# Kernel optimization log

Measured on AMD Instinct MI355X. Metric: run time of the kernel, lower is better.

## Reference

```python
import jax, jax.numpy as jnp
import numpy as np

B, T, C, H = 2, 2048, 1024, 16
D = C // H  # head dim = 64

def setup_inputs() -> dict:
    key = jax.random.key(0)
    ks = jax.random.split(key, 5)
    s = 0.02
    return {
        "x": jax.random.normal(ks[0], (B, T, C), dtype=jnp.float32),
        "Wqkv": jax.random.normal(ks[1], (C, 3 * C), dtype=jnp.float32) * s,
        "bqkv": jnp.zeros((3 * C,), dtype=jnp.float32),
        "Wproj": jax.random.normal(ks[2], (C, C), dtype=jnp.float32) * s,
        "bproj": jnp.zeros((C,), dtype=jnp.float32),
    }

def reference(x, Wqkv, bqkv, Wproj, bproj):
    b, t, c = x.shape
    qkv = x @ Wqkv + bqkv                       # [B,T,3C]
    q, k, v = jnp.split(qkv, 3, axis=-1)
    # [B,T,C] -> [B,H,T,D]
    q = q.reshape(b, t, H, D).transpose(0, 2, 1, 3)
    k = k.reshape(b, t, H, D).transpose(0, 2, 1, 3)
    v = v.reshape(b, t, H, D).transpose(0, 2, 1, 3)
    scale = 1.0 / np.sqrt(D).astype(np.float32)
    attn = jnp.einsum('bhqd,bhkd->bhqk', q, k) * scale  # [B,H,T,T]
    causal = jnp.tril(jnp.ones((t, t), dtype=bool))
    attn = jnp.where(causal, attn, jnp.float32(-jnp.inf))
    attn = jax.nn.softmax(attn, axis=-1)
    y = jnp.einsum('bhqk,bhkd->bhqd', attn, v)          # [B,H,T,D]
    y = y.transpose(0, 2, 1, 3).reshape(b, t, c)        # [B,T,C]
    return y @ Wproj + bproj
```

## Files before the change

kernel.cpp:

```cpp
#include <hip/hip_runtime.h>
#include <stdint.h>

#define B_ 2
#define T_ 2048
#define C_ 1024
#define H_ 16
#define D_ 64
#define M_ (B_*T_)
#define BHTD_ (B_*H_*T_*D_)

typedef __bf16 bf16x8 __attribute__((ext_vector_type(8)));
typedef __bf16 bf16x4 __attribute__((ext_vector_type(4)));
typedef float f32x4 __attribute__((ext_vector_type(4)));

static __device__ __forceinline__ unsigned short f32_bf16(float f) {
    unsigned int u = __float_as_uint(f);
    u += 0x7FFFu + ((u >> 16) & 1u);
    return (unsigned short)(u >> 16);
}

__global__ void prep_kernel(const float* __restrict__ x, unsigned short* __restrict__ xbf,
                            const float* __restrict__ Wqkv, unsigned short* __restrict__ wqkv_t,
                            const float* __restrict__ Wproj, unsigned short* __restrict__ wproj_t) {
    __shared__ float tile[32][33];
    const int id = blockIdx.x;
    const int tid = threadIdx.x;
    if (id < 4096) {
        int i = (id * 256 + tid) * 4;
        float4 f = *(const float4*)(x + i);
        ushort4 o;
        o.x = f32_bf16(f.x); o.y = f32_bf16(f.y); o.z = f32_bf16(f.z); o.w = f32_bf16(f.w);
        *(ushort4*)(xbf + i) = o;
        return;
    }
    const float* W; unsigned short* Wt; int K, N, bx, by;
    if (id < 7168) {
        int r = id - 4096; W = Wqkv; Wt = wqkv_t; K = 1024; N = 3072;
        bx = r % 96; by = r / 96;
    } else {
        int r = id - 7168; W = Wproj; Wt = wproj_t; K = 1024; N = 1024;
        bx = r & 31; by = r >> 5;
    }
    int n0 = bx * 32, k0 = by * 32;
    int tx = tid & 31, ty = tid >> 5;
    #pragma unroll
    for (int j = 0; j < 32; j += 8)
        tile[ty + j][tx] = W[(size_t)(k0 + ty + j) * N + n0 + tx];
    __syncthreads();
    #pragma unroll
    for (int j = 0; j < 32; j += 8)
        Wt[(size_t)(n0 + ty + j) * K + k0 + tx] = f32_bf16(tile[tx][ty + j]);
}

template<int EPI, int BN>
__global__ __launch_bounds__(256) void gemm_bt(
    const unsigned short* __restrict__ A,
    const unsigned short* __restrict__ Bt,
    const float* __restrict__ bias,
    unsigned short* __restrict__ out_bf16,
    float* __restrict__ out_f32,
    int M, int N, int K)
{
    constexpr int NI = (BN == 128) ? 4 : 2;
    constexpr int BSTR = BN * 32;
    __shared__ __align__(16) unsigned short smem[16640];
    unsigned short* AsU = smem;
    unsigned short* BsU = smem + 8192;
    int tid = threadIdx.x;
    int lane = tid & 63, wid = tid >> 6;
    int fr = lane & 15, fg = lane >> 4;
    int row0 = blockIdx.x * 128, col0 = blockIdx.y * BN;
    int wm = (wid >> 1) * 64, wn = (wid & 1) * (BN / 2);

    f32x4 acc[4][NI];
    #pragma unroll
    for (int i = 0; i < 4; ++i)
        #pragma unroll
        for (int j = 0; j < NI; ++j)
            acc[i][j] = (f32x4){0.f, 0.f, 0.f, 0.f};

    const int srw = lane >> 2;
    const int scl = (lane & 3) * 8;
    const int c0 = wid * 2, c1 = wid * 2 + 1;

    auto stage = [&](int buf, int k0) {
        __builtin_amdgcn_global_load_lds(
            (const __attribute__((address_space(1))) void*)(A + (size_t)(row0 + c0 * 16 + srw) * K + k0 + scl),
            (__attribute__((address_space(3))) void*)(AsU + buf * 4096 + c0 * 512), 16, 0, 0);
        __builtin_amdgcn_global_load_lds(
            (const __attribute__((address_space(1))) void*)(A + (size_t)(row0 + c1 * 16 + srw) * K + k0 + scl),
            (__attribute__((address_space(3))) void*)(AsU + buf * 4096 + c1 * 512), 16, 0, 0);
        if (BN == 128) {
            __builtin_amdgcn_global_load_lds(
                (const __attribute__((address_space(1))) void*)(Bt + (size_t)(col0 + c0 * 16 + srw) * K + k0 + scl),
                (__attribute__((address_space(3))) void*)(BsU + buf * BSTR + c0 * 512), 16, 0, 0);
            __builtin_amdgcn_global_load_lds(
                (const __attribute__((address_space(1))) void*)(Bt + (size_t)(col0 + c1 * 16 + srw) * K + k0 + scl),
                (__attribute__((address_space(3))) void*)(BsU + buf * BSTR + c1 * 512), 16, 0, 0);
        } else {
            __builtin_amdgcn_global_load_lds(
                (const __attribute__((address_space(1))) void*)(Bt + (size_t)(col0 + wid * 16 + srw) * K + k0 + scl),
                (__attribute__((address_space(3))) void*)(BsU + buf * BSTR + wid * 512), 16, 0, 0);
        }
    };

    stage(0, 0);
    __syncthreads();

    int cur = 0;
    for (int k0 = 0; k0 < K; k0 += 32) {
        if (k0 + 32 < K) stage(cur ^ 1, k0 + 32);

        bf16x8 af[4], bfr[NI];
        #pragma unroll
        for (int i = 0; i < 4; ++i)
            af[i] = *(const bf16x8*)(AsU + cur * 4096 + (wm + i * 16 + fr) * 32 + fg * 8);
        #pragma unroll
        for (int i = 0; i < NI; ++i)
            bfr[i] = *(const bf16x8*)(BsU + cur * BSTR + (wn + i * 16 + fr) * 32 + fg * 8);
        #pragma unroll
        for (int mi = 0; mi < 4; ++mi)
            #pragma unroll
            for (int ni = 0; ni < NI; ++ni)
                acc[mi][ni] = __builtin_amdgcn_mfma_f32_16x16x32_bf16(af[mi], bfr[ni], acc[mi][ni], 0, 0, 0);

        __syncthreads();
        cur ^= 1;
    }

    if (EPI == 0 && BN == 128 && col0 >= 2048) {
        #pragma unroll
        for (int ni = 0; ni < NI; ++ni) {
            const int cl = wn + ni * 16 + fr;
            const float bv = bias[col0 + cl];
            #pragma unroll
            for (int mi = 0; mi < 4; ++mi) {
                const int rl = wm + mi * 16 + fg * 4;
                bf16x4 pk = {(__bf16)(acc[mi][ni][0] + bv), (__bf16)(acc[mi][ni][1] + bv),
                             (__bf16)(acc[mi][ni][2] + bv), (__bf16)(acc[mi][ni][3] + bv)};
                uint2 w = __builtin_bit_cast(uint2, pk);
                *(unsigned int*)(smem + cl * 130 + rl)     = w.x;
                *(unsigned int*)(smem + cl * 130 + rl + 2) = w.y;
            }
        }
        __syncthreads();
        const int c = tid >> 1, half = tid & 1;
        const int col = col0 + c;
        const int d = col & 63, h2 = (col >> 6) & 15;
        const int bb = row0 >> 11;
        const int t0 = (row0 & 2047) + half * 64;
        unsigned short* dst = out_bf16 + (size_t)2 * BHTD_ +
                              ((size_t)(bb * H_ + h2) * D_ + d) * T_ + t0;
        const unsigned short* src = smem + c * 130 + half * 64;
        #pragma unroll
        for (int j = 0; j < 8; ++j) {
            uint4 v;
            v.x = *(const unsigned int*)(src + j * 8 + 0);
            v.y = *(const unsigned int*)(src + j * 8 + 2);
            v.z = *(const unsigned int*)(src + j * 8 + 4);
            v.w = *(const unsigned int*)(src + j * 8 + 6);
            *(uint4*)(dst + j * 8) = v;
        }
        return;
    }

    #pragma unroll
    for (int mi = 0; mi < 4; ++mi) {
        int rowb = row0 + wm + mi * 16 + fg * 4;
        #pragma unroll
        for (int ni = 0; ni < NI; ++ni) {
            int col = col0 + wn + ni * 16 + fr;
            float bv = bias[col];
            #pragma unroll
            for (int r = 0; r < 4; ++r) {
                float v = acc[mi][ni][r] + bv;
                int rr = rowb + r;
                if (EPI == 0) {
                    int part = col >> 10, c = col & 1023;
                    int h = c >> 6, d = c & 63;
                    int b = rr >> 11, t = rr & 2047;
                    if (part == 0) v *= 0.18033688011112042f;
                    size_t idx = (size_t)part * BHTD_ + ((size_t)(b * H_ + h) * T_ + t) * D_ + d;
                    out_bf16[idx] = f32_bf16(v);
                } else {
                    out_f32[(size_t)rr * N + col] = v;
                }
            }
        }
    }
}

__global__ __launch_bounds__(256) void attn_kernel(
    const unsigned short* __restrict__ qg,
    const unsigned short* __restrict__ kg,
    const unsigned short* __restrict__ vtg,
    unsigned short* __restrict__ y)
{
    const int id = blockIdx.x;
    const int xcd = id & 7, loc = id >> 3;
    const int bh = xcd * 4 + (loc & 3);
    const int iq0 = loc >> 2;
    const int iq = (iq0 < 8) ? iq0 : 23 - iq0;
    const int chlo = iq, chhi = 31 - iq;
    const int b = bh >> 4, h = bh & 15;
    const int tid = threadIdx.x, wid = tid >> 6, lane = tid & 63;
    const int fr = lane & 15, fg = lane >> 4;

    const unsigned short* qp = qg + (size_t)bh * (T_ * D_);
    const unsigned short* kp = kg + (size_t)bh * (T_ * D_);
    const unsigned short* vp = vtg + (size_t)bh * (D_ * T_);

    __shared__ __align__(16) char Ks[2][64 * 128];
    __shared__ __align__(16) char Vs[2][64 * 128];
    __shared__ __align__(16) char Ps[4][32 * 128];
    char* Pw = Ps[wid];

    const int rhi = chhi * 64 + wid * 16;
    const int rlo = chlo * 64 + wid * 16;

    const int srow = tid >> 3;
    const int scb  = (tid & 7) * 16;
    const int sws  = scb ^ ((srow & 7) << 4);

    bf16x8 qhi[2], qlo[2];
    #pragma unroll
    for (int kd = 0; kd < 2; ++kd) {
        qhi[kd] = *(const bf16x8*)(qp + (size_t)(rhi + fr) * D_ + kd * 32 + fg * 8);
        qlo[kd] = *(const bf16x8*)(qp + (size_t)(rlo + fr) * D_ + kd * 32 + fg * 8);
    }

    f32x4 oHi[4], oLo[4];
    float lHi = 0.f, lLo = 0.f;
    #pragma unroll
    for (int n = 0; n < 4; ++n) {
        oHi[n] = (f32x4){0.f, 0.f, 0.f, 0.f};
        oLo[n] = (f32x4){0.f, 0.f, 0.f, 0.f};
    }

    const int ntk  = chhi + 1;
    const int ntlo = chlo + 1;

    {
        uint4 k0 = *(const uint4*)(kp + (size_t)srow        * D_ + (scb >> 1));
        uint4 k1 = *(const uint4*)(kp + (size_t)(srow + 32) * D_ + (scb >> 1));
        uint4 v0 = *(const uint4*)(vp + (size_t)srow        * T_ + (scb >> 1));
        uint4 v1 = *(const uint4*)(vp + (size_t)(srow + 32) * T_ + (scb >> 1));
        *(uint4*)(Ks[0] + srow * 128 + sws)        = k0;
        *(uint4*)(Ks[0] + (srow + 32) * 128 + sws) = k1;
        *(uint4*)(Vs[0] + srow * 128 + sws)        = v0;
        *(uint4*)(Vs[0] + (srow + 32) * 128 + sws) = v1;
    }
    __syncthreads();

    int cur = 0;
    for (int t = 0; t < ntk; ++t) {
        const int kv0 = t * 64;
        const int kv1 = (t + 1 < ntk) ? kv0 + 64 : kv0;

        uint4 pk0 = *(const uint4*)(kp + (size_t)(kv1 + srow)      * D_ + (scb >> 1));
        uint4 pk1 = *(const uint4*)(kp + (size_t)(kv1 + srow + 32) * D_ + (scb >> 1));
        uint4 pv0 = *(const uint4*)(vp + (size_t)srow        * T_ + kv1 + (scb >> 1));
        uint4 pv1 = *(const uint4*)(vp + (size_t)(srow + 32) * T_ + kv1 + (scb >> 1));

        const char* Kb = Ks[cur];
        const char* Vb = Vs[cur];
        const unsigned lsw = (unsigned)((fr & 7) << 4);
        const bool lo_act = (t < ntlo);

        f32x4 sh[4], sl[4];
        #pragma unroll
        for (int n = 0; n < 4; ++n) {
            sh[n] = (f32x4){0.f, 0.f, 0.f, 0.f};
            sl[n] = (f32x4){0.f, 0.f, 0.f, 0.f};
        }
        __builtin_amdgcn_s_setprio(1);
        #pragma unroll
        for (int kd = 0; kd < 2; ++kd)
            #pragma unroll
            for (int n = 0; n < 4; ++n) {
                bf16x8 kf = *(const bf16x8*)(Kb + (n * 16 + fr) * 128 +
                                             (((unsigned)(kd * 64 + fg * 16)) ^ lsw));
                sh[n] = __builtin_amdgcn_mfma_f32_16x16x32_bf16(kf, qhi[kd], sh[n], 0, 0, 0);
                if (lo_act)
                    sl[n] = __builtin_amdgcn_mfma_f32_16x16x32_bf16(kf, qlo[kd], sl[n], 0, 0, 0);
            }
        __builtin_amdgcn_s_setprio(0);

        bf16x8 vf[4][2];
        #pragma unroll
        for (int nd = 0; nd < 4; ++nd)
            #pragma unroll
            for (int kk = 0; kk < 2; ++kk)
                vf[nd][kk] = *(const bf16x8*)(Vb + (nd * 16 + fr) * 128 +
                                              (((unsigned)(kk * 64 + fg * 16)) ^ lsw));

        {
            const bool masked = (t == chhi);
            const int qrow = rhi + fr;
            const unsigned prow = (unsigned)fr * 128;
            #pragma unroll
            for (int n = 0; n < 4; ++n) {
                float x0 = sh[n][0], x1 = sh[n][1], x2 = sh[n][2], x3 = sh[n][3];
                if (masked) {
                    const int kvb = kv0 + n * 16 + fg * 4;
                    if (kvb     > qrow) x0 = -1e30f;
                    if (kvb + 1 > qrow) x1 = -1e30f;
                    if (kvb + 2 > qrow) x2 = -1e30f;
                    if (kvb + 3 > qrow) x3 = -1e30f;
                }
                const float p0 = exp2f(x0), p1 = exp2f(x1);
                const float p2 = exp2f(x2), p3 = exp2f(x3);
                lHi += (p0 + p1) + (p2 + p3);
                bf16x4 pk4 = {(__bf16)p0, (__bf16)p1, (__bf16)p2, (__bf16)p3};
                *(uint2*)(Pw + ((prow + (unsigned)(n * 32 + fg * 8)) ^ lsw)) =
                    __builtin_bit_cast(uint2, pk4);
            }
        }
        {
            const unsigned prow = (unsigned)fr * 128;
            __builtin_amdgcn_s_setprio(1);
            #pragma unroll
            for (int kk = 0; kk < 2; ++kk) {
                bf16x8 pb = *(const bf16x8*)(Pw + ((prow + (unsigned)(kk * 64 + fg * 16)) ^ lsw));
                #pragma unroll
                for (int nd = 0; nd < 4; ++nd)
                    oHi[nd] = __builtin_amdgcn_mfma_f32_16x16x32_bf16(vf[nd][kk], pb, oHi[nd], 0, 0, 0);
            }
            __builtin_amdgcn_s_setprio(0);
        }
        if (lo_act) {
            const bool masked = (t == chlo);
            const int qrow = rlo + fr;
            const unsigned prow = (unsigned)(16 + fr) * 128;
            #pragma unroll
            for (int n = 0; n < 4; ++n) {
                float x0 = sl[n][0], x1 = sl[n][1], x2 = sl[n][2], x3 = sl[n][3];
                if (masked) {
                    const int kvb = kv0 + n * 16 + fg * 4;
                    if (kvb     > qrow) x0 = -1e30f;
                    if (kvb + 1 > qrow) x1 = -1e30f;
                    if (kvb + 2 > qrow) x2 = -1e30f;
                    if (kvb + 3 > qrow) x3 = -1e30f;
                }
                const float p0 = exp2f(x0), p1 = exp2f(x1);
                const float p2 = exp2f(x2), p3 = exp2f(x3);
                lLo += (p0 + p1) + (p2 + p3);
                bf16x4 pk4 = {(__bf16)p0, (__bf16)p1, (__bf16)p2, (__bf16)p3};
                *(uint2*)(Pw + ((prow + (unsigned)(n * 32 + fg * 8)) ^ lsw)) =
                    __builtin_bit_cast(uint2, pk4);
            }
            const unsigned prow2 = (unsigned)(16 + fr) * 128;
            __builtin_amdgcn_s_setprio(1);
            #pragma unroll
            for (int kk = 0; kk < 2; ++kk) {
                bf16x8 pb = *(const bf16x8*)(Pw + ((prow2 + (unsigned)(kk * 64 + fg * 16)) ^ lsw));
                #pragma unroll
                for (int nd = 0; nd < 4; ++nd)
                    oLo[nd] = __builtin_amdgcn_mfma_f32_16x16x32_bf16(vf[nd][kk], pb, oLo[nd], 0, 0, 0);
            }
            __builtin_amdgcn_s_setprio(0);
        }

        {
            char* Kn = Ks[cur ^ 1];
            char* Vn = Vs[cur ^ 1];
            *(uint4*)(Kn + srow * 128 + sws)        = pk0;
            *(uint4*)(Kn + (srow + 32) * 128 + sws) = pk1;
            *(uint4*)(Vn + srow * 128 + sws)        = pv0;
            *(uint4*)(Vn + (srow + 32) * 128 + sws) = pv1;
        }
        __syncthreads();
        cur ^= 1;
    }

    #pragma unroll
    for (int s = 0; s < 2; ++s) {
        float rs = s ? lLo : lHi;
        rs += __shfl_xor(rs, 16);
        rs += __shfl_xor(rs, 32);
        const float inv = 1.f / rs;
        const int trow = (s ? rlo : rhi) + fr;
        f32x4* oT = s ? oLo : oHi;
        #pragma unroll
        for (int nd = 0; nd < 4; ++nd) {
            bf16x4 ov = {(__bf16)(oT[nd][0] * inv), (__bf16)(oT[nd][1] * inv),
                         (__bf16)(oT[nd][2] * inv), (__bf16)(oT[nd][3] * inv)};
            *(uint2*)(y + ((size_t)b * T_ + trow) * C_ + h * 64 + nd * 16 + fg * 4) =
                __builtin_bit_cast(uint2, ov);
        }
    }
}

extern "C" void kernel_launch(void* const* d_in, const int* in_sizes, int n_in,
                              void* d_out, int out_size, void* d_ws, size_t ws_size,
                              hipStream_t stream) {
    const float* x     = (const float*)d_in[0];
    const float* Wqkv  = (const float*)d_in[1];
    const float* bqkv  = (const float*)d_in[2];
    const float* Wproj = (const float*)d_in[3];
    const float* bproj = (const float*)d_in[4];
    float* out = (float*)d_out;

    char* ws = (char*)d_ws;
    unsigned short* x_bf    = (unsigned short*)(ws);
    unsigned short* wqkv_t  = (unsigned short*)(ws + 8388608);
    unsigned short* wproj_t = (unsigned short*)(ws + 14680064);
    unsigned short* qkv     = (unsigned short*)(ws + 16777216);
    unsigned short* ybuf    = (unsigned short*)(ws + 41943040);

    prep_kernel<<<dim3(8192), 256, 0, stream>>>(x, x_bf, Wqkv, wqkv_t, Wproj, wproj_t);

    gemm_bt<0, 128><<<dim3(M_ / 128, 3072 / 128), 256, 0, stream>>>(
        x_bf, wqkv_t, bqkv, qkv, nullptr, M_, 3072, 1024);

    attn_kernel<<<dim3(512), 256, 0, stream>>>(
        qkv, qkv + (size_t)BHTD_, qkv + 2 * (size_t)BHTD_, ybuf);

    gemm_bt<1, 64><<<dim3(M_ / 128, 1024 / 64), 256, 0, stream>>>(
        ybuf, wproj_t, bproj, nullptr, out, M_, 1024, 1024);
}
```

Before: 119.5 us.

## Rewrite attention with 32x32 MFMA, register P via permlane swap, direct-to-LDS loads

The attention kernel moves from 16x16x32 MFMA tiles to 32x32x16 MFMA tiles. P is kept in registers and rearranged with permlane32_swap instead of a round trip through shared memory. K/V staging now uses global_load_lds so tiles go straight into LDS without passing through registers, and the block shrinks to 128 threads with two waves each covering 32 query rows. The query-tile ordering also changes. This aims to cut LDS traffic and register staging, at the cost of fewer waves per block and possibly lower occupancy.

```diff
diff --git a/kernel.cpp b/kernel.cpp
--- a/kernel.cpp
+++ b/kernel.cpp
@@ -11,12 +11,19 @@
 
 typedef __bf16 bf16x8 __attribute__((ext_vector_type(8)));
 typedef __bf16 bf16x4 __attribute__((ext_vector_type(4)));
+typedef __bf16 bf16x2 __attribute__((ext_vector_type(2)));
 typedef float f32x4 __attribute__((ext_vector_type(4)));
+typedef float f32x16 __attribute__((ext_vector_type(16)));
 
 static __device__ __forceinline__ unsigned short f32_bf16(float f) {
     unsigned int u = __float_as_uint(f);
     u += 0x7FFFu + ((u >> 16) & 1u);
     return (unsigned short)(u >> 16);
+}
+
+static __device__ __forceinline__ int pack_bf16_2(float a, float b) {
+    bf16x2 v = {(__bf16)a, (__bf16)b};
+    return __builtin_bit_cast(int, v);
 }
 
 __global__ void prep_kernel(const float* __restrict__ x, unsigned short* __restrict__ xbf,
@@ -190,7 +197,7 @@
     }
 }
 
-__global__ __launch_bounds__(256) void attn_kernel(
+__global__ __launch_bounds__(128, 1) void attn_kernel(
     const unsigned short* __restrict__ qg,
     const unsigned short* __restrict__ kg,
     const unsigned short* __restrict__ vtg,
@@ -199,194 +206,185 @@
     const int id = blockIdx.x;
     const int xcd = id & 7, loc = id >> 3;
     const int bh = xcd * 4 + (loc & 3);
-    const int iq0 = loc >> 2;
-    const int iq = (iq0 < 8) ? iq0 : 23 - iq0;
-    const int chlo = iq, chhi = 31 - iq;
+    const int iq = loc >> 2;
+    const int chhi = 31 - iq, chlo = iq;
     const int b = bh >> 4, h = bh & 15;
     const int tid = threadIdx.x, wid = tid >> 6, lane = tid & 63;
-    const int fr = lane & 15, fg = lane >> 4;
+    const int lq = lane & 31, hi = lane >> 5;
 
     const unsigned short* qp = qg + (size_t)bh * (T_ * D_);
-    const unsigned short* kp = kg + (size_t)bh * (T_ * D_);
-    const unsigned short* vp = vtg + (size_t)bh * (D_ * T_);
-
-    __shared__ __align__(16) char Ks[2][64 * 128];
-    __shared__ __align__(16) char Vs[2][64 * 128];
-    __shared__ __align__(16) char Ps[4][32 * 128];
-    char* Pw = Ps[wid];
-
-    const int rhi = chhi * 64 + wid * 16;
-    const int rlo = chlo * 64 + wid * 16;
-
-    const int srow = tid >> 3;
-    const int scb  = (tid & 7) * 16;
-    const int sws  = scb ^ ((srow & 7) << 4);
-
-    bf16x8 qhi[2], qlo[2];
-    #pragma unroll
-    for (int kd = 0; kd < 2; ++kd) {
-        qhi[kd] = *(const bf16x8*)(qp + (size_t)(rhi + fr) * D_ + kd * 32 + fg * 8);
-        qlo[kd] = *(const bf16x8*)(qp + (size_t)(rlo + fr) * D_ + kd * 32 + fg * 8);
-    }
-
-    f32x4 oHi[4], oLo[4];
-    float lHi = 0.f, lLo = 0.f;
-    #pragma unroll
-    for (int n = 0; n < 4; ++n) {
-        oHi[n] = (f32x4){0.f, 0.f, 0.f, 0.f};
-        oLo[n] = (f32x4){0.f, 0.f, 0.f, 0.f};
-    }
-
-    const int ntk  = chhi + 1;
-    const int ntlo = chlo + 1;
-
-    {
-        uint4 k0 = *(const uint4*)(kp + (size_t)srow        * D_ + (scb >> 1));
-        uint4 k1 = *(const uint4*)(kp + (size_t)(srow + 32) * D_ + (scb >> 1));
-        uint4 v0 = *(const uint4*)(vp + (size_t)srow        * T_ + (scb >> 1));
-        uint4 v1 = *(const uint4*)(vp + (size_t)(srow + 32) * T_ + (scb >> 1));
-        *(uint4*)(Ks[0] + srow * 128 + sws)        = k0;
-        *(uint4*)(Ks[0] + (srow + 32) * 128 + sws) = k1;
-        *(uint4*)(Vs[0] + srow * 128 + sws)        = v0;
-        *(uint4*)(Vs[0] + (srow + 32) * 128 + sws) = v1;
-    }
+    const char* kpB = (const char*)(kg + (size_t)bh * (T_ * D_));
+    const char* vpB = (const char*)(vtg + (size_t)bh * (D_ * T_));
+
+    __shared__ __align__(16) char Ks[2][8192];
+    __shared__ __align__(16) char Vs[2][8192];
+
+    const int rhi = chhi * 64 + wid * 32;
+    const int rlo = chlo * 64 + wid * 32;
+    const int ntk = chhi + 1, ntlo = chlo + 1;
+
+    bf16x8 qh[4], ql[4];
+    #pragma unroll
+    for (int ds = 0; ds < 4; ++ds) {
+        qh[ds] = *(const bf16x8*)(qp + (size_t)(rhi + lq) * D_ + ds * 16 + hi * 8);
+        ql[ds] = *(const bf16x8*)(qp + (size_t)(rlo + lq) * D_ + ds * 16 + hi * 8);
+    }
+
+    f32x16 oh0, oh1, ol0, ol1;
+    #pragma unroll
+    for (int e = 0; e < 16; ++e) { oh0[e] = 0.f; oh1[e] = 0.f; ol0[e] = 0.f; ol1[e] = 0.f; }
+    float lh = 0.f, ll = 0.f;
+
+    const int srow8 = lane >> 3;
+    const int scol  = (lane & 7) * 16;
+    const int ssw   = srow8 << 4;
+
+    auto stage = [&](int buf, int kv0) {
+        #pragma unroll
+        for (int blk = 0; blk < 4; ++blk) {
+            const int rbase = wid * 32 + blk * 8;
+            __builtin_amdgcn_global_load_lds(
+                (const __attribute__((address_space(1))) void*)
+                    (kpB + (size_t)(kv0 + rbase + srow8) * 128 + (scol ^ ssw)),
+                (__attribute__((address_space(3))) void*)(Ks[buf] + rbase * 128), 16, 0, 0);
+            __builtin_amdgcn_global_load_lds(
+                (const __attribute__((address_space(1))) void*)
+                    (vpB + (size_t)(rbase + srow8) * 4096 + kv0 * 2 + (scol ^ ssw)),
+                (__attribute__((address_space(3))) void*)(Vs[buf] + rbase * 128), 16, 0, 0);
+        }
+    };
+
+    auto make_pb = [&](const f32x16& p4, int g4a) -> bf16x8 {
+        int A0 = pack_bf16_2(p4[g4a * 4 + 0], p4[g4a * 4 + 1]);
+        int A1 = pack_bf16_2(p4[g4a * 4 + 2], p4[g4a * 4 + 3]);
+        int B0 = pack_bf16_2(p4[g4a * 4 + 4], p4[g4a * 4 + 5]);
+        int B1 = pack_bf16_2(p4[g4a * 4 + 6], p4[g4a * 4 + 7]);
+        auto ra = __builtin_amdgcn_permlane32_swap(A0, B0, false, false);
+        auto rb = __builtin_amdgcn_permlane32_swap(A1, B1, false, false);
+        int4 w;
+        w.x = ra[0]; w.y = rb[0]; w.z = ra[1]; w.w = rb[1];
+        return __builtin_bit_cast(bf16x8, w);
+    };
+
+    stage(0, 0);
     __syncthreads();
 
+    const int lsw = (lq & 7) << 4;
     int cur = 0;
     for (int t = 0; t < ntk; ++t) {
         const int kv0 = t * 64;
-        const int kv1 = (t + 1 < ntk) ? kv0 + 64 : kv0;
-
-        uint4 pk0 = *(const uint4*)(kp + (size_t)(kv1 + srow)      * D_ + (scb >> 1));
-        uint4 pk1 = *(const uint4*)(kp + (size_t)(kv1 + srow + 32) * D_ + (scb >> 1));
-        uint4 pv0 = *(const uint4*)(vp + (size_t)srow        * T_ + kv1 + (scb >> 1));
-        uint4 pv1 = *(const uint4*)(vp + (size_t)(srow + 32) * T_ + kv1 + (scb >> 1));
+        if (t + 1 < ntk) stage(cur ^ 1, kv0 + 64);
 
         const char* Kb = Ks[cur];
         const char* Vb = Vs[cur];
-        const unsigned lsw = (unsigned)((fr & 7) << 4);
         const bool lo_act = (t < ntlo);
 
-        f32x4 sh[4], sl[4];
-        #pragma unroll
-        for (int n = 0; n < 4; ++n) {
-            sh[n] = (f32x4){0.f, 0.f, 0.f, 0.f};
-            sl[n] = (f32x4){0.f, 0.f, 0.f, 0.f};
-        }
-        __builtin_amdgcn_s_setprio(1);
-        #pragma unroll
-        for (int kd = 0; kd < 2; ++kd)
-            #pragma unroll
-            for (int n = 0; n < 4; ++n) {
-                bf16x8 kf = *(const bf16x8*)(Kb + (n * 16 + fr) * 128 +
-                                             (((unsigned)(kd * 64 + fg * 16)) ^ lsw));
-                sh[n] = __builtin_amdgcn_mfma_f32_16x16x32_bf16(kf, qhi[kd], sh[n], 0, 0, 0);
-                if (lo_act)
-                    sl[n] = __builtin_amdgcn_mfma_f32_16x16x32_bf16(kf, qlo[kd], sl[n], 0, 0, 0);
-            }
-        __builtin_amdgcn_s_setprio(0);
-
-        bf16x8 vf[4][2];
-        #pragma unroll
-        for (int nd = 0; nd < 4; ++nd)
-            #pragma unroll
-            for (int kk = 0; kk < 2; ++kk)
-                vf[nd][kk] = *(const bf16x8*)(Vb + (nd * 16 + fr) * 128 +
-                                              (((unsigned)(kk * 64 + fg * 16)) ^ lsw));
+        f32x16 sh0, sh1, sl0, sl1;
+        #pragma unroll
+        for (int e = 0; e < 16; ++e) { sh0[e] = 0.f; sh1[e] = 0.f; sl0[e] = 0.f; sl1[e] = 0.f; }
+        #pragma unroll
+        for (int ds = 0; ds < 4; ++ds) {
+            bf16x8 kfA = *(const bf16x8*)(Kb + lq * 128        + ((ds * 32 + hi * 16) ^ lsw));
+            bf16x8 kfB = *(const bf16x8*)(Kb + (32 + lq) * 128 + ((ds * 32 + hi * 16) ^ lsw));
+            sh0 = __builtin_amdgcn_mfma_f32_32x32x16_bf16(kfA, qh[ds], sh0, 0, 0, 0);
+            sh1 = __builtin_amdgcn_mfma_f32_32x32x16_bf16(kfB, qh[ds], sh1, 0, 0, 0);
+            if (lo_act) {
+                sl0 = __builtin_amdgcn_mfma_f32_32x32x16_bf16(kfA, ql[ds], sl0, 0, 0, 0);
+                sl1 = __builtin_amdgcn_mfma_f32_32x32x16_bf16(kfB, ql[ds], sl1, 0, 0, 0);
+            }
+        }
+
+        bf16x8 vf[2][4];
+        #pragma unroll
+        for (int dd = 0; dd < 2; ++dd)
+            #pragma unroll
+            for (int st = 0; st < 4; ++st)
+                vf[dd][st] = *(const bf16x8*)(Vb + (dd * 32 + lq) * 128 +
+                                              ((st * 32 + hi * 16) ^ lsw));
 
         {
-            const bool masked = (t == chhi);
-            const int qrow = rhi + fr;
-            const unsigned prow = (unsigned)fr * 128;
-            #pragma unroll
-            for (int n = 0; n < 4; ++n) {
-                float x0 = sh[n][0], x1 = sh[n][1], x2 = sh[n][2], x3 = sh[n][3];
-                if (masked) {
-                    const int kvb = kv0 + n * 16 + fg * 4;
-                    if (kvb     > qrow) x0 = -1e30f;
-                    if (kvb + 1 > qrow) x1 = -1e30f;
-                    if (kvb + 2 > qrow) x2 = -1e30f;
-                    if (kvb + 3 > qrow) x3 = -1e30f;
+            const bool diag = (t == chhi);
+            const int qrow = rhi + lq;
+            if (diag) {
+                #pragma unroll
+                for (int e = 0; e < 16; ++e) {
+                    const int kvl = (e & 3) + ((e >> 2) << 3) + hi * 4;
+                    sh0[e] = exp2f((kv0 + kvl <= qrow) ? sh0[e] : -1e30f);
+                    sh1[e] = exp2f((kv0 + 32 + kvl <= qrow) ? sh1[e] : -1e30f);
                 }
-                const float p0 = exp2f(x0), p1 = exp2f(x1);
-                const float p2 = exp2f(x2), p3 = exp2f(x3);
-                lHi += (p0 + p1) + (p2 + p3);
-                bf16x4 pk4 = {(__bf16)p0, (__bf16)p1, (__bf16)p2, (__bf16)p3};
-                *(uint2*)(Pw + ((prow + (unsigned)(n * 32 + fg * 8)) ^ lsw)) =
-                    __builtin_bit_cast(uint2, pk4);
-            }
-        }
-        {
-            const unsigned prow = (unsigned)fr * 128;
-            __builtin_amdgcn_s_setprio(1);
-            #pragma unroll
-            for (int kk = 0; kk < 2; ++kk) {
-                bf16x8 pb = *(const bf16x8*)(Pw + ((prow + (unsigned)(kk * 64 + fg * 16)) ^ lsw));
+            } else {
                 #pragma unroll
-                for (int nd = 0; nd < 4; ++nd)
-                    oHi[nd] = __builtin_amdgcn_mfma_f32_16x16x32_bf16(vf[nd][kk], pb, oHi[nd], 0, 0, 0);
-            }
-            __builtin_amdgcn_s_setprio(0);
+                for (int e = 0; e < 16; ++e) { sh0[e] = exp2f(sh0[e]); sh1[e] = exp2f(sh1[e]); }
+            }
+            float a0 = 0.f;
+            #pragma unroll
+            for (int e = 0; e < 16; ++e) a0 += sh0[e] + sh1[e];
+            lh += a0;
+            bf16x8 pb = make_pb(sh0, 0);
+            oh0 = __builtin_amdgcn_mfma_f32_32x32x16_bf16(vf[0][0], pb, oh0, 0, 0, 0);
+            oh1 = __builtin_amdgcn_mfma_f32_32x32x16_bf16(vf[1][0], pb, oh1, 0, 0, 0);
+            pb = make_pb(sh0, 2);
+            oh0 = __builtin_amdgcn_mfma_f32_32x32x16_bf16(vf[0][1], pb, oh0, 0, 0, 0);
+            oh1 = __builtin_amdgcn_mfma_f32_32x32x16_bf16(vf[1][1], pb, oh1, 0, 0, 0);
+            pb = make_pb(sh1, 0);
+            oh0 = __builtin_amdgcn_mfma_f32_32x32x16_bf16(vf[0][2], pb, oh0, 0, 0, 0);
+            oh1 = __builtin_amdgcn_mfma_f32_32x32x16_bf16(vf[1][2], pb, oh1, 0, 0, 0);
+            pb = make_pb(sh1, 2);
+            oh0 = __builtin_amdgcn_mfma_f32_32x32x16_bf16(vf[0][3], pb, oh0, 0, 0, 0);
+            oh1 = __builtin_amdgcn_mfma_f32_32x32x16_bf16(vf[1][3], pb, oh1, 0, 0, 0);
         }
         if (lo_act) {
-            const bool masked = (t == chlo);
-            const int qrow = rlo + fr;
-            const unsigned prow = (unsigned)(16 + fr) * 128;
-            #pragma unroll
-            for (int n = 0; n < 4; ++n) {
-                float x0 = sl[n][0], x1 = sl[n][1], x2 = sl[n][2], x3 = sl[n][3];
-                if (masked) {
-                    const int kvb = kv0 + n * 16 + fg * 4;
-                    if (kvb     > qrow) x0 = -1e30f;
-                    if (kvb + 1 > qrow) x1 = -1e30f;
-                    if (kvb + 2 > qrow) x2 = -1e30f;
-                    if (kvb + 3 > qrow) x3 = -1e30f;
+            const bool diag = (t == chlo);
+            const int qrow = rlo + lq;
+            if (diag) {
+                #pragma unroll
+                for (int e = 0; e < 16; ++e) {
+                    const int kvl = (e & 3) + ((e >> 2) << 3) + hi * 4;
+                    sl0[e] = exp2f((kv0 + kvl <= qrow) ? sl0[e] : -1e30f);
+                    sl1[e] = exp2f((kv0 + 32 + kvl <= qrow) ? sl1[e] : -1e30f);
                 }
-                const float p0 = exp2f(x0), p1 = exp2f(x1);
-                const float p2 = exp2f(x2), p3 = exp2f(x3);
-                lLo += (p0 + p1) + (p2 + p3);
-                bf16x4 pk4 = {(__bf16)p0, (__bf16)p1, (__bf16)p2, (__bf16)p3};
-                *(uint2*)(Pw + ((prow + (unsigned)(n * 32 + fg * 8)) ^ lsw)) =
-                    __builtin_bit_cast(uint2, pk4);
-            }
-            const unsigned prow2 = (unsigned)(16 + fr) * 128;
-            __builtin_amdgcn_s_setprio(1);
-            #pragma unroll
-            for (int kk = 0; kk < 2; ++kk) {
-                bf16x8 pb = *(const bf16x8*)(Pw + ((prow2 + (unsigned)(kk * 64 + fg * 16)) ^ lsw));
+            } else {
                 #pragma unroll
-                for (int nd = 0; nd < 4; ++nd)
-                    oLo[nd] = __builtin_amdgcn_mfma_f32_16x16x32_bf16(vf[nd][kk], pb, oLo[nd], 0, 0, 0);
-            }
-            __builtin_amdgcn_s_setprio(0);
-        }
-
-        {
-            char* Kn = Ks[cur ^ 1];
-            char* Vn = Vs[cur ^ 1];
-            *(uint4*)(Kn + srow * 128 + sws)        = pk0;
-            *(uint4*)(Kn + (srow + 32) * 128 + sws) = pk1;
-            *(uint4*)(Vn + srow * 128 + sws)        = pv0;
-            *(uint4*)(Vn + (srow + 32) * 128 + sws) = pv1;
-        }
+                for (int e = 0; e < 16; ++e) { sl0[e] = exp2f(sl0[e]); sl1[e] = exp2f(sl1[e]); }
+            }
+            float a0 = 0.f;
+            #pragma unroll
+            for (int e = 0; e < 16; ++e) a0 += sl0[e] + sl1[e];
+            ll += a0;
+            bf16x8 pb = make_pb(sl0, 0);
+            ol0 = __builtin_amdgcn_mfma_f32_32x32x16_bf16(vf[0][0], pb, ol0, 0, 0, 0);
+            ol1 = __builtin_amdgcn_mfma_f32_32x32x16_bf16(vf[1][0], pb, ol1, 0, 0, 0);
+            pb = make_pb(sl0, 2);
+            ol0 = __builtin_amdgcn_mfma_f32_32x32x16_bf16(vf[0][1], pb, ol0, 0, 0, 0);
+            ol1 = __builtin_amdgcn_mfma_f32_32x32x16_bf16(vf[1][1], pb, ol1, 0, 0, 0);
+            pb = make_pb(sl1, 0);
+            ol0 = __builtin_amdgcn_mfma_f32_32x32x16_bf16(vf[0][2], pb, ol0, 0, 0, 0);
+            ol1 = __builtin_amdgcn_mfma_f32_32x32x16_bf16(vf[1][2], pb, ol1, 0, 0, 0);
+            pb = make_pb(sl1, 2);
+            ol0 = __builtin_amdgcn_mfma_f32_32x32x16_bf16(vf[0][3], pb, ol0, 0, 0, 0);
+            ol1 = __builtin_amdgcn_mfma_f32_32x32x16_bf16(vf[1][3], pb, ol1, 0, 0, 0);
+        }
+
         __syncthreads();
         cur ^= 1;
     }
 
     #pragma unroll
     for (int s = 0; s < 2; ++s) {
-        float rs = s ? lLo : lHi;
-        rs += __shfl_xor(rs, 16);
-        rs += __shfl_xor(rs, 32);
-        const float inv = 1.f / rs;
-        const int trow = (s ? rlo : rhi) + fr;
-        f32x4* oT = s ? oLo : oHi;
-        #pragma unroll
-        for (int nd = 0; nd < 4; ++nd) {
-            bf16x4 ov = {(__bf16)(oT[nd][0] * inv), (__bf16)(oT[nd][1] * inv),
-                         (__bf16)(oT[nd][2] * inv), (__bf16)(oT[nd][3] * inv)};
-            *(uint2*)(y + ((size_t)b * T_ + trow) * C_ + h * 64 + nd * 16 + fg * 4) =
-                __builtin_bit_cast(uint2, ov);
+        float lr = s ? ll : lh;
+        lr += __shfl_xor(lr, 32);
+        const float inv = 1.f / lr;
+        const int trow = (s ? rlo : rhi) + lq;
+        unsigned short* yrow = y + ((size_t)b * T_ + trow) * C_ + h * 64;
+        #pragma unroll
+        for (int dd = 0; dd < 2; ++dd) {
+            const f32x16& o = s ? (dd ? ol1 : ol0) : (dd ? oh1 : oh0);
+            #pragma unroll
+            for (int g4 = 0; g4 < 4; ++g4) {
+                bf16x4 ov = {(__bf16)(o[g4 * 4 + 0] * inv), (__bf16)(o[g4 * 4 + 1] * inv),
+                             (__bf16)(o[g4 * 4 + 2] * inv), (__bf16)(o[g4 * 4 + 3] * inv)};
+                *(uint2*)(yrow + dd * 32 + g4 * 8 + hi * 4) = __builtin_bit_cast(uint2, ov);
+            }
         }
     }
 }
@@ -413,7 +411,7 @@
     gemm_bt<0, 128><<<dim3(M_ / 128, 3072 / 128), 256, 0, stream>>>(
         x_bf, wqkv_t, bqkv, qkv, nullptr, M_, 3072, 1024);
 
-    attn_kernel<<<dim3(512), 256, 0, stream>>>(
+    attn_kernel<<<dim3(512), 128, 0, stream>>>(
         qkv, qkv + (size_t)BHTD_, qkv + 2 * (size_t)BHTD_, ybuf);
 
     gemm_bt<1, 64><<<dim3(M_ / 128, 1024 / 64), 256, 0, stream>>>(
```

Measured after the change: 127.8 us. 1.07x slower.

## Stage attention K/V tiles with direct global-to-LDS loads and use hardware exp2

Applied to the files above, without the earlier changes.

The attention kernel's K and V double-buffer staging now uses global_load_lds straight into shared memory, replacing register-staged loads followed by LDS stores. The XOR swizzle is applied on the global source address, so the LDS layout the MFMA reads expect is unchanged. This removes the VGPRs that held prefetched tiles and the explicit LDS write instructions, at the cost of relying on the async DMA path being finished at the existing barrier. The softmax exp2f calls are also replaced with the native __builtin_amdgcn_exp2f intrinsic to drop range-handling overhead.

```diff
diff --git a/kernel.cpp b/kernel.cpp
--- a/kernel.cpp
+++ b/kernel.cpp
@@ -8,6 +8,9 @@
 #define D_ 64
 #define M_ (B_*T_)
 #define BHTD_ (B_*H_*T_*D_)
+
+#define AS1 __attribute__((address_space(1)))
+#define AS3 __attribute__((address_space(3)))
 
 typedef __bf16 bf16x8 __attribute__((ext_vector_type(8)));
 typedef __bf16 bf16x4 __attribute__((ext_vector_type(4)));
@@ -85,22 +88,22 @@
 
     auto stage = [&](int buf, int k0) {
         __builtin_amdgcn_global_load_lds(
-            (const __attribute__((address_space(1))) void*)(A + (size_t)(row0 + c0 * 16 + srw) * K + k0 + scl),
-            (__attribute__((address_space(3))) void*)(AsU + buf * 4096 + c0 * 512), 16, 0, 0);
+            (const AS1 void*)(A + (size_t)(row0 + c0 * 16 + srw) * K + k0 + scl),
+            (AS3 void*)(AsU + buf * 4096 + c0 * 512), 16, 0, 0);
         __builtin_amdgcn_global_load_lds(
-            (const __attribute__((address_space(1))) void*)(A + (size_t)(row0 + c1 * 16 + srw) * K + k0 + scl),
-            (__attribute__((address_space(3))) void*)(AsU + buf * 4096 + c1 * 512), 16, 0, 0);
+            (const AS1 void*)(A + (size_t)(row0 + c1 * 16 + srw) * K + k0 + scl),
+            (AS3 void*)(AsU + buf * 4096 + c1 * 512), 16, 0, 0);
         if (BN == 128) {
             __builtin_amdgcn_global_load_lds(
-                (const __attribute__((address_space(1))) void*)(Bt + (size_t)(col0 + c0 * 16 + srw) * K + k0 + scl),
-                (__attribute__((address_space(3))) void*)(BsU + buf * BSTR + c0 * 512), 16, 0, 0);
+                (const AS1 void*)(Bt + (size_t)(col0 + c0 * 16 + srw) * K + k0 + scl),
+                (AS3 void*)(BsU + buf * BSTR + c0 * 512), 16, 0, 0);
             __builtin_amdgcn_global_load_lds(
-                (const __attribute__((address_space(1))) void*)(Bt + (size_t)(col0 + c1 * 16 + srw) * K + k0 + scl),
-                (__attribute__((address_space(3))) void*)(BsU + buf * BSTR + c1 * 512), 16, 0, 0);
+                (const AS1 void*)(Bt + (size_t)(col0 + c1 * 16 + srw) * K + k0 + scl),
+                (AS3 void*)(BsU + buf * BSTR + c1 * 512), 16, 0, 0);
         } else {
             __builtin_amdgcn_global_load_lds(
-                (const __attribute__((address_space(1))) void*)(Bt + (size_t)(col0 + wid * 16 + srw) * K + k0 + scl),
-                (__attribute__((address_space(3))) void*)(BsU + buf * BSTR + wid * 512), 16, 0, 0);
+                (const AS1 void*)(Bt + (size_t)(col0 + wid * 16 + srw) * K + k0 + scl),
+                (AS3 void*)(BsU + buf * BSTR + wid * 512), 16, 0, 0);
         }
     };
 
@@ -207,20 +210,16 @@
     const int fr = lane & 15, fg = lane >> 4;
 
     const unsigned short* qp = qg + (size_t)bh * (T_ * D_);
-    const unsigned short* kp = kg + (size_t)bh * (T_ * D_);
-    const unsigned short* vp = vtg + (size_t)bh * (D_ * T_);
-
-    __shared__ __align__(16) char Ks[2][64 * 128];
-    __shared__ __align__(16) char Vs[2][64 * 128];
+    const char* kpB = (const char*)(kg + (size_t)bh * (T_ * D_));
+    const char* vpB = (const char*)(vtg + (size_t)bh * (D_ * T_));
+
+    __shared__ __align__(16) char Ks[2][8192];
+    __shared__ __align__(16) char Vs[2][8192];
     __shared__ __align__(16) char Ps[4][32 * 128];
     char* Pw = Ps[wid];
 
     const int rhi = chhi * 64 + wid * 16;
     const int rlo = chlo * 64 + wid * 16;
-
-    const int srow = tid >> 3;
-    const int scb  = (tid & 7) * 16;
-    const int sws  = scb ^ ((srow & 7) << 4);
 
     bf16x8 qhi[2], qlo[2];
     #pragma unroll
@@ -240,31 +239,34 @@
     const int ntk  = chhi + 1;
     const int ntlo = chlo + 1;
 
-    {
-        uint4 k0 = *(const uint4*)(kp + (size_t)srow        * D_ + (scb >> 1));
-        uint4 k1 = *(const uint4*)(kp + (size_t)(srow + 32) * D_ + (scb >> 1));
-        uint4 v0 = *(const uint4*)(vp + (size_t)srow        * T_ + (scb >> 1));
-        uint4 v1 = *(const uint4*)(vp + (size_t)(srow + 32) * T_ + (scb >> 1));
-        *(uint4*)(Ks[0] + srow * 128 + sws)        = k0;
-        *(uint4*)(Ks[0] + (srow + 32) * 128 + sws) = k1;
-        *(uint4*)(Vs[0] + srow * 128 + sws)        = v0;
-        *(uint4*)(Vs[0] + (srow + 32) * 128 + sws) = v1;
-    }
+    const int srow8 = lane >> 3;
+    const int scol  = (lane & 7) * 16;
+    const int ssw   = srow8 << 4;
+
+    auto stage = [&](int buf, int kv0) {
+        #pragma unroll
+        for (int bc = 0; bc < 2; ++bc) {
+            const int rbase = wid * 16 + bc * 8;
+            __builtin_amdgcn_global_load_lds(
+                (const AS1 void*)(kpB + (size_t)(kv0 + rbase + srow8) * 128 + (scol ^ ssw)),
+                (AS3 void*)(Ks[buf] + rbase * 128), 16, 0, 0);
+            __builtin_amdgcn_global_load_lds(
+                (const AS1 void*)(vpB + (size_t)(rbase + srow8) * 4096 + (size_t)kv0 * 2 + (scol ^ ssw)),
+                (AS3 void*)(Vs[buf] + rbase * 128), 16, 0, 0);
+        }
+    };
+
+    stage(0, 0);
     __syncthreads();
 
+    const unsigned lsw = (unsigned)((fr & 7) << 4);
     int cur = 0;
     for (int t = 0; t < ntk; ++t) {
         const int kv0 = t * 64;
-        const int kv1 = (t + 1 < ntk) ? kv0 + 64 : kv0;
-
-        uint4 pk0 = *(const uint4*)(kp + (size_t)(kv1 + srow)      * D_ + (scb >> 1));
-        uint4 pk1 = *(const uint4*)(kp + (size_t)(kv1 + srow + 32) * D_ + (scb >> 1));
-        uint4 pv0 = *(const uint4*)(vp + (size_t)srow        * T_ + kv1 + (scb >> 1));
-        uint4 pv1 = *(const uint4*)(vp + (size_t)(srow + 32) * T_ + kv1 + (scb >> 1));
+        if (t + 1 < ntk) stage(cur ^ 1, kv0 + 64);
 
         const char* Kb = Ks[cur];
         const char* Vb = Vs[cur];
-        const unsigned lsw = (unsigned)((fr & 7) << 4);
         const bool lo_act = (t < ntlo);
 
         f32x4 sh[4], sl[4];
@@ -308,8 +310,10 @@
                     if (kvb + 2 > qrow) x2 = -1e30f;
                     if (kvb + 3 > qrow) x3 = -1e30f;
                 }
-                const float p0 = exp2f(x0), p1 = exp2f(x1);
-                const float p2 = exp2f(x2), p3 = exp2f(x3);
+                const float p0 = __builtin_amdgcn_exp2f(x0);
+                const float p1 = __builtin_amdgcn_exp2f(x1);
+                const float p2 = __builtin_amdgcn_exp2f(x2);
+                const float p3 = __builtin_amdgcn_exp2f(x3);
                 lHi += (p0 + p1) + (p2 + p3);
                 bf16x4 pk4 = {(__bf16)p0, (__bf16)p1, (__bf16)p2, (__bf16)p3};
                 *(uint2*)(Pw + ((prow + (unsigned)(n * 32 + fg * 8)) ^ lsw)) =
@@ -342,18 +346,19 @@
                     if (kvb + 2 > qrow) x2 = -1e30f;
                     if (kvb + 3 > qrow) x3 = -1e30f;
                 }
-                const float p0 = exp2f(x0), p1 = exp2f(x1);
-                const float p2 = exp2f(x2), p3 = exp2f(x3);
+                const float p0 = __builtin_amdgcn_exp2f(x0);
+                const float p1 = __builtin_amdgcn_exp2f(x1);
+                const float p2 = __builtin_amdgcn_exp2f(x2);
+                const float p3 = __builtin_amdgcn_exp2f(x3);
                 lLo += (p0 + p1) + (p2 + p3);
                 bf16x4 pk4 = {(__bf16)p0, (__bf16)p1, (__bf16)p2, (__bf16)p3};
                 *(uint2*)(Pw + ((prow + (unsigned)(n * 32 + fg * 8)) ^ lsw)) =
                     __builtin_bit_cast(uint2, pk4);
             }
-            const unsigned prow2 = (unsigned)(16 + fr) * 128;
             __builtin_amdgcn_s_setprio(1);
             #pragma unroll
             for (int kk = 0; kk < 2; ++kk) {
-                bf16x8 pb = *(const bf16x8*)(Pw + ((prow2 + (unsigned)(kk * 64 + fg * 16)) ^ lsw));
+                bf16x8 pb = *(const bf16x8*)(Pw + ((prow + (unsigned)(kk * 64 + fg * 16)) ^ lsw));
                 #pragma unroll
                 for (int nd = 0; nd < 4; ++nd)
                     oLo[nd] = __builtin_amdgcn_mfma_f32_16x16x32_bf16(vf[nd][kk], pb, oLo[nd], 0, 0, 0);
@@ -361,14 +366,6 @@
             __builtin_amdgcn_s_setprio(0);
         }
 
-        {
-            char* Kn = Ks[cur ^ 1];
-            char* Vn = Vs[cur ^ 1];
-            *(uint4*)(Kn + srow * 128 + sws)        = pk0;
-            *(uint4*)(Kn + (srow + 32) * 128 + sws) = pk1;
-            *(uint4*)(Vn + srow * 128 + sws)        = pv0;
-            *(uint4*)(Vn + (srow + 32) * 128 + sws) = pv1;
-        }
         __syncthreads();
         cur ^= 1;
     }
```

After: 117.3 us. No clear change (-1.8%).
